# Performance work log

Hardware: AMD Instinct MI355X
Metric: run time of the kernel (lower is better)

Reference implementation:

```python
import jax, jax.numpy as jnp
import numpy as np

T, B, D, H, L = 1024, 64, 512, 512, 2


def setup_inputs() -> dict:
    key = jax.random.key(0)
    ks = jax.random.split(key, 10)
    s = 1.0 / np.sqrt(D)
    return {
        "x": jax.random.normal(ks[0], (T, B, D), jnp.float32),
        "hidden": jax.random.normal(ks[1], (L, B, H), jnp.float32),
        "fc_w": jax.random.normal(ks[2], (D, D), jnp.float32) * s,
        "fc_b": jax.random.normal(ks[3], (D,), jnp.float32) * s,
        "w0": jax.random.normal(ks[4], (H, D), jnp.float32) * s,
        "b0": jax.random.normal(ks[5], (H,), jnp.float32) * s,
        "u0": jax.random.uniform(ks[6], (H,), jnp.float32, -1.0, 1.0),
        "w1": jax.random.normal(ks[7], (H, H), jnp.float32) * s,
        "b1": jax.random.normal(ks[8], (H,), jnp.float32) * s,
        "u1": jax.random.uniform(ks[9], (H,), jnp.float32, -1.0, 1.0),
    }


def _indrnn_layer(inp, h0, w, b, u):
    # Precompute input projection for all timesteps: [T, B, H]
    pre = jnp.einsum("tbd,hd->tbh", inp, w) + b

    def step(h, p):
        h_new = jax.nn.relu(p + u * h)  # elementwise recurrent weight
        return h_new, h_new

    h_last, outs = jax.lax.scan(step, h0, pre)
    return outs, h_last


def reference(x, hidden, fc_w, fc_b, w0, b0, u0, w1, b1, u1):
    # fc layer before the IndRNN stack
    x = jnp.einsum("tbd,ed->tbe", x, fc_w) + fc_b
    out0, h0 = _indrnn_layer(x, hidden[0], w0, b0, u0)
    out1, h1 = _indrnn_layer(out0, hidden[1], w1, b1, u1)
    hn = jnp.stack([h0, h1], axis=0)  # [L, B, H]
    return out1, hn
```

## Files before the change

### kernel.cpp

```cpp
#include <hip/hip_runtime.h>
#include <hip/hip_bf16.h>
#include <cstdint>
#include <cstddef>

#define T_DIM 1024
#define B_DIM 64
#define D_DIM 512
#define H_DIM 512
#define TBROWS (T_DIM * B_DIM)
#define BH (B_DIM * H_DIM)
#define TBH ((size_t)T_DIM * (size_t)BH)

typedef __bf16 bf16x8 __attribute__((ext_vector_type(8)));
typedef float floatx4 __attribute__((ext_vector_type(4)));

__device__ __forceinline__ void async_load16(const void* g, void* l) {
  __builtin_amdgcn_global_load_lds(
      (const __attribute__((address_space(1))) unsigned int*)g,
      (__attribute__((address_space(3))) unsigned int*)l,
      16, 0, 0);
}

__device__ __forceinline__ void wait_vm(int n) {
  switch (n) {
    case 16: asm volatile("s_waitcnt vmcnt(16)" ::: "memory"); break;
    case 24: asm volatile("s_waitcnt vmcnt(24)" ::: "memory"); break;
    case 32: asm volatile("s_waitcnt vmcnt(32)" ::: "memory"); break;
    case 40: asm volatile("s_waitcnt vmcnt(40)" ::: "memory"); break;
    case 48: asm volatile("s_waitcnt vmcnt(48)" ::: "memory"); break;
    default: asm volatile("s_waitcnt vmcnt(0)" ::: "memory"); break;
  }
}

__global__ __launch_bounds__(256) void prep_kernel(
    const float* __restrict__ w0, const float* __restrict__ fc_w,
    const float* __restrict__ fc_b, const float* __restrict__ b0,
    const float* __restrict__ w1, __bf16* __restrict__ Wc,
    __bf16* __restrict__ w1bf, float* __restrict__ bcomb) {
  const int blk = blockIdx.x;
  const int tid = threadIdx.x;
  if (blk < 128) {
    const int h0 = (blk >> 1) * 8;
    const int d = ((blk & 1) << 8) + tid;
    float a[8];
#pragma unroll
    for (int j = 0; j < 8; j++) a[j] = 0.f;
#pragma unroll 4
    for (int e = 0; e < D_DIM; ++e) {
      const float fv = fc_w[(size_t)e * D_DIM + d];
#pragma unroll
      for (int j = 0; j < 8; j++)
        a[j] = fmaf(w0[(size_t)(h0 + j) * D_DIM + e], fv, a[j]);
    }
#pragma unroll
    for (int j = 0; j < 8; j++)
      Wc[(size_t)(h0 + j) * D_DIM + d] = (__bf16)a[j];
  } else if (blk < 256) {
    const long i = ((long)(blk - 128) * 256 + tid) * 8;
    const float4 a = *(const float4*)(w1 + i);
    const float4 b = *(const float4*)(w1 + i + 4);
    bf16x8 v;
    v[0] = (__bf16)a.x; v[1] = (__bf16)a.y; v[2] = (__bf16)a.z; v[3] = (__bf16)a.w;
    v[4] = (__bf16)b.x; v[5] = (__bf16)b.y; v[6] = (__bf16)b.z; v[7] = (__bf16)b.w;
    *(bf16x8*)(w1bf + i) = v;
  } else {
    const int h = (blk - 256) * 256 + tid;
    float acc = b0[h];
    const float4* w4 = (const float4*)(w0 + (size_t)h * D_DIM);
#pragma unroll 4
    for (int e = 0; e < D_DIM / 4; ++e) {
      const float4 wv = w4[e];
      acc = fmaf(wv.x, fc_b[e * 4 + 0], acc);
      acc = fmaf(wv.y, fc_b[e * 4 + 1], acc);
      acc = fmaf(wv.z, fc_b[e * 4 + 2], acc);
      acc = fmaf(wv.w, fc_b[e * 4 + 3], acc);
    }
    bcomb[h] = acc;
  }
}

#define BM 128
#define BN 128
#define BK 32

__device__ __forceinline__ int xcd_swizzle(int bid, int nwg) {
  return (bid & 7) * (nwg >> 3) + (bid >> 3);
}

__global__ __launch_bounds__(256) void gemm_a32_bt_bias(
    const float* __restrict__ A,
    const __bf16* __restrict__ Bm,
    const float* __restrict__ bias,
    __bf16* __restrict__ C,
    int M, int N, int K) {
  __shared__ float Asf[2][BM * BK];
  __shared__ __bf16 Bs[2][BN * BK];

  const int tid = threadIdx.x;
  const int lane = tid & 63;
  const int wave = tid >> 6;
  const int wg = xcd_swizzle((int)blockIdx.x, (int)gridDim.x);
  const int nb = N / BN;
  const int bm = wg / nb;
  const int bn = wg % nb;
  const int m0 = bm * BM, n0 = bn * BN;

  floatx4 zero = {0.f, 0.f, 0.f, 0.f};
  floatx4 acc[4][4];
#pragma unroll
  for (int i = 0; i < 4; i++)
#pragma unroll
    for (int j = 0; j < 4; j++) acc[i][j] = zero;

  const int e0 = (wave * 2 + 0) * 64 + lane;
  const int e1 = (wave * 2 + 1) * 64 + lane;
  const int r0 = e0 >> 2, g0 = (e0 & 3) ^ ((r0 >> 1) & 3);
  const int r1 = e1 >> 2, g1 = (e1 & 3) ^ ((r1 >> 1) & 3);

  const int tm = (wave >> 1) * 64;
  const int tn = (wave & 1) * 64;
  const int lrow = lane & 15;
  const int lk = (lane >> 4) * 8;
  const int sB = lk >> 3;
  const int s0 = lk >> 2;

  const int ea = wave * 4;

  const int KT = K / BK;

  auto stage = [&](int b, int k0) {
#pragma unroll
    for (int i = 0; i < 4; i++) {
      const int e = (ea + i) * 64 + lane;
      const int r = e >> 3;
      const int g = (e & 7) ^ (r & 7);
      async_load16(&A[(size_t)(m0 + r) * K + k0 + g * 4],
                   &Asf[b][(ea + i) * 256]);
    }
    async_load16(&Bm[(size_t)(n0 + r0) * K + k0 + g0 * 8],
                 &Bs[b][(wave * 2 + 0) * 512]);
    async_load16(&Bm[(size_t)(n0 + r1) * K + k0 + g1 * 8],
                 &Bs[b][(wave * 2 + 1) * 512]);
  };

  stage(0, 0);
  __syncthreads();

  int cur = 0;
  for (int kt = 0; kt < KT; ++kt) {
    if (kt + 1 < KT) stage(cur ^ 1, (kt + 1) * BK);

    bf16x8 af[4], bfr[4];
#pragma unroll
    for (int i = 0; i < 4; i++) {
      const int ra = tm + i * 16 + lrow;
      const int k7 = ra & 7;
      const float4 fa = *(const float4*)&Asf[cur][ra * 32 + ((s0 ^ k7) << 2)];
      const float4 fb = *(const float4*)&Asf[cur][ra * 32 + (((s0 + 1) ^ k7) << 2)];
      bf16x8 v;
      v[0] = (__bf16)fa.x; v[1] = (__bf16)fa.y; v[2] = (__bf16)fa.z; v[3] = (__bf16)fa.w;
      v[4] = (__bf16)fb.x; v[5] = (__bf16)fb.y; v[6] = (__bf16)fb.z; v[7] = (__bf16)fb.w;
      af[i] = v;
      const int rb = tn + i * 16 + lrow;
      bfr[i] = *(const bf16x8*)&Bs[cur][rb * 32 + ((sB ^ ((rb >> 1) & 3)) << 3)];
    }
#pragma unroll
    for (int i = 0; i < 4; i++)
#pragma unroll
      for (int j = 0; j < 4; j++)
        acc[i][j] = __builtin_amdgcn_mfma_f32_16x16x32_bf16(af[i], bfr[j],
                                                            acc[i][j], 0, 0, 0);
    __syncthreads();
    cur ^= 1;
  }

  const int ccol = lane & 15;
  const int crow = (lane >> 4) * 4;
  float bv[4];
#pragma unroll
  for (int j = 0; j < 4; j++) bv[j] = bias[n0 + tn + j * 16 + ccol];
#pragma unroll
  for (int i = 0; i < 4; i++) {
#pragma unroll
    for (int j = 0; j < 4; j++) {
      const size_t base =
          (size_t)(m0 + tm + i * 16 + crow) * N + (n0 + tn + j * 16 + ccol);
#pragma unroll
      for (int r = 0; r < 4; r++)
        C[base + (size_t)r * N] = (__bf16)(acc[i][j][r] + bv[j]);
    }
  }
}

__global__ __launch_bounds__(256) void gemm_bt_bias(
    const __bf16* __restrict__ A,
    const __bf16* __restrict__ Bm,
    const float* __restrict__ bias,
    __bf16* __restrict__ C,
    int M, int N, int K) {
  __shared__ __bf16 As[2][BM * BK];
  __shared__ __bf16 Bs[2][BN * BK];

  const int tid = threadIdx.x;
  const int lane = tid & 63;
  const int wave = tid >> 6;
  const int wg = xcd_swizzle((int)blockIdx.x, (int)gridDim.x);
  const int nb = N / BN;
  const int bm = wg / nb;
  const int bn = wg % nb;
  const int m0 = bm * BM, n0 = bn * BN;

  floatx4 zero = {0.f, 0.f, 0.f, 0.f};
  floatx4 acc[4][4];
#pragma unroll
  for (int i = 0; i < 4; i++)
#pragma unroll
    for (int j = 0; j < 4; j++) acc[i][j] = zero;

  const int e0 = (wave * 2 + 0) * 64 + lane;
  const int e1 = (wave * 2 + 1) * 64 + lane;
  const int r0 = e0 >> 2, g0 = (e0 & 3) ^ ((r0 >> 1) & 3);
  const int r1 = e1 >> 2, g1 = (e1 & 3) ^ ((r1 >> 1) & 3);

  const int tm = (wave >> 1) * 64;
  const int tn = (wave & 1) * 64;
  const int lrow = lane & 15;
  const int lk = (lane >> 4) * 8;
  const int sB = lk >> 3;

  const int KT = K / BK;

  auto stage = [&](int b, int k0) {
    async_load16(&A[(size_t)(m0 + r0) * K + k0 + g0 * 8],
                 &As[b][(wave * 2 + 0) * 512]);
    async_load16(&A[(size_t)(m0 + r1) * K + k0 + g1 * 8],
                 &As[b][(wave * 2 + 1) * 512]);
    async_load16(&Bm[(size_t)(n0 + r0) * K + k0 + g0 * 8],
                 &Bs[b][(wave * 2 + 0) * 512]);
    async_load16(&Bm[(size_t)(n0 + r1) * K + k0 + g1 * 8],
                 &Bs[b][(wave * 2 + 1) * 512]);
  };

  stage(0, 0);
  __syncthreads();

  int cur = 0;
  for (int kt = 0; kt < KT; ++kt) {
    if (kt + 1 < KT) stage(cur ^ 1, (kt + 1) * BK);

    bf16x8 af[4], bfr[4];
#pragma unroll
    for (int i = 0; i < 4; i++) {
      const int ra = tm + i * 16 + lrow;
      const int rb = tn + i * 16 + lrow;
      af[i]  = *(const bf16x8*)&As[cur][ra * 32 + ((sB ^ ((ra >> 1) & 3)) << 3)];
      bfr[i] = *(const bf16x8*)&Bs[cur][rb * 32 + ((sB ^ ((rb >> 1) & 3)) << 3)];
    }
#pragma unroll
    for (int i = 0; i < 4; i++)
#pragma unroll
      for (int j = 0; j < 4; j++)
        acc[i][j] = __builtin_amdgcn_mfma_f32_16x16x32_bf16(af[i], bfr[j],
                                                            acc[i][j], 0, 0, 0);
    __syncthreads();
    cur ^= 1;
  }

  const int ccol = lane & 15;
  const int crow = (lane >> 4) * 4;
  float bv[4];
#pragma unroll
  for (int j = 0; j < 4; j++) bv[j] = bias[n0 + tn + j * 16 + ccol];
#pragma unroll
  for (int i = 0; i < 4; i++) {
#pragma unroll
    for (int j = 0; j < 4; j++) {
      const size_t base =
          (size_t)(m0 + tm + i * 16 + crow) * N + (n0 + tn + j * 16 + ccol);
#pragma unroll
      for (int r = 0; r < 4; r++)
        C[base + (size_t)r * N] = (__bf16)(acc[i][j][r] + bv[j]);
    }
  }
}

#define TS 64
#define NTILE (T_DIM / TS)

template <bool BF16OUT>
__global__ __launch_bounds__(64, 1) void scan_kernel(
    const __bf16* __restrict__ pre,
    const float* __restrict__ h0,
    const float* __restrict__ u,
    void* __restrict__ outp,
    float* __restrict__ hn) {
  constexpr int OBYTES = BF16OUT ? 2 : 4;
  __shared__ __bf16 tin[3][TS * 64];
  __shared__ char oraw[2][TS * 64 * OBYTES];

  const int lane = threadIdx.x;
  const int c0 = blockIdx.x * 64;
  const int idx = c0 + lane;
  const float uu = u[idx & (H_DIM - 1)];
  float h = h0[idx];

  const int lrow = lane >> 3;
  const int lcg = (lane & 7) * 8;

#pragma unroll
  for (int i = 0; i < 8; i++)
    async_load16(&pre[(size_t)(i * 8 + lrow) * BH + c0 + lcg], &tin[0][i * 512]);
#pragma unroll
  for (int i = 0; i < 8; i++)
    async_load16(&pre[(size_t)(TS + i * 8 + lrow) * BH + c0 + lcg],
                 &tin[1][i * 512]);

  for (int tile = 0; tile < NTILE; ++tile) {
    __builtin_amdgcn_sched_barrier(0);
    if (tile + 2 < NTILE) {
      const int nb = (tile + 2) % 3;
      const size_t nt0 = (size_t)(tile + 2) * TS;
#pragma unroll
      for (int i = 0; i < 8; i++)
        async_load16(&pre[(nt0 + i * 8 + lrow) * BH + c0 + lcg],
                     &tin[nb][i * 512]);
    }
    int wv;
    if (BF16OUT)
      wv = (tile == 0 || tile == NTILE - 1) ? 16
         : (tile == 1 || tile == NTILE - 2) ? 24 : 32;
    else
      wv = (tile == 0) ? 16
         : (tile == 1 || tile == NTILE - 1) ? 32
         : (tile == NTILE - 2) ? 40 : 48;
    wait_vm(wv);
    __builtin_amdgcn_sched_barrier(0);

    const int buf = tile % 3;
    const int t0 = tile * TS;
    char* ob = oraw[tile & 1];
#pragma unroll
    for (int s = 0; s < TS; s++) {
      const float p = (float)tin[buf][s * 64 + lane];
      h = fmaxf(fmaf(uu, h, p), 0.0f);
      if (BF16OUT) ((__bf16*)ob)[s * 64 + lane] = (__bf16)h;
      else         ((float*)ob)[s * 64 + lane] = h;
    }
    if (BF16OUT) {
#pragma unroll
      for (int i = 0; i < 8; i++) {
        const int row = i * 8 + (lane >> 3);
        const bf16x8 v =
            *(const bf16x8*)&((const __bf16*)ob)[row * 64 + (lane & 7) * 8];
        *(bf16x8*)&((__bf16*)outp)[(size_t)(t0 + row) * BH + c0 + (lane & 7) * 8] = v;
      }
    } else {
#pragma unroll
      for (int i = 0; i < 16; i++) {
        const int row = i * 4 + (lane >> 4);
        const float4 v =
            *(const float4*)&((const float*)ob)[row * 64 + (lane & 15) * 4];
        *(float4*)&((float*)outp)[(size_t)(t0 + row) * BH + c0 + (lane & 15) * 4] = v;
      }
    }
  }
  hn[idx] = h;
}

extern "C" void kernel_launch(void* const* d_in, const int* in_sizes, int n_in,
                              void* d_out, int out_size, void* d_ws,
                              size_t ws_size, hipStream_t stream) {
  (void)in_sizes; (void)n_in; (void)out_size; (void)ws_size;
  const float* x      = (const float*)d_in[0];
  const float* hidden = (const float*)d_in[1];
  const float* fc_w   = (const float*)d_in[2];
  const float* fc_b   = (const float*)d_in[3];
  const float* w0     = (const float*)d_in[4];
  const float* b0     = (const float*)d_in[5];
  const float* u0     = (const float*)d_in[6];
  const float* w1     = (const float*)d_in[7];
  const float* b1     = (const float*)d_in[8];
  const float* u1     = (const float*)d_in[9];
  float* out = (float*)d_out;

  char* ws = (char*)d_ws;
  __bf16* pre  = (__bf16*)ws;
  __bf16* out0 = (__bf16*)(ws + TBH * 2);
  char*   tail = ws + 2 * TBH * 2;
  __bf16* Wc    = (__bf16*)tail;
  __bf16* w1bf  = (__bf16*)(tail + 512 * 1024);
  float*  bcomb = (float*)(tail + 1024 * 1024);

  float* hn = out + TBH;

  prep_kernel<<<258, 256, 0, stream>>>(w0, fc_w, fc_b, b0, w1, Wc, w1bf, bcomb);
  gemm_a32_bt_bias<<<(TBROWS / BM) * (H_DIM / BN), 256, 0, stream>>>(
      x, Wc, bcomb, pre, TBROWS, H_DIM, D_DIM);
  scan_kernel<true><<<BH / 64, 64, 0, stream>>>(pre, hidden, u0, (void*)out0, hn);
  gemm_bt_bias<<<(TBROWS / BM) * (H_DIM / BN), 256, 0, stream>>>(
      out0, w1bf, b1, pre, TBROWS, H_DIM, H_DIM);
  scan_kernel<false><<<BH / 64, 64, 0, stream>>>(pre, hidden + BH, u1,
                                                 (void*)out, hn + BH);
}
```

Measured before the change: 450.7 us.

## Triple-buffer GEMM K-loop with async prefetch depth of two

Both projection GEMMs move from double to triple buffering in LDS. Tiles are prefetched two iterations ahead, and partial s_waitcnt vmcnt counts let the newest loads stay in flight while the current tile is consumed. Raw s_barrier plus sched_barrier replace __syncthreads so the compiler cannot reorder around the waits. This adds LDS use, which can lower occupancy (fp32 A tiles now need 48KB+24KB), and it relies on hand-set vmcnt values being correct.

```diff
diff --git a/kernel.cpp b/kernel.cpp
--- a/kernel.cpp
+++ b/kernel.cpp
@@ -23,12 +23,16 @@
 
 __device__ __forceinline__ void wait_vm(int n) {
   switch (n) {
+    case 4:  asm volatile("s_waitcnt vmcnt(4)"  ::: "memory"); break;
+    case 6:  asm volatile("s_waitcnt vmcnt(6)"  ::: "memory"); break;
+    case 8:  asm volatile("s_waitcnt vmcnt(8)"  ::: "memory"); break;
+    case 12: asm volatile("s_waitcnt vmcnt(12)" ::: "memory"); break;
     case 16: asm volatile("s_waitcnt vmcnt(16)" ::: "memory"); break;
     case 24: asm volatile("s_waitcnt vmcnt(24)" ::: "memory"); break;
     case 32: asm volatile("s_waitcnt vmcnt(32)" ::: "memory"); break;
     case 40: asm volatile("s_waitcnt vmcnt(40)" ::: "memory"); break;
     case 48: asm volatile("s_waitcnt vmcnt(48)" ::: "memory"); break;
-    default: asm volatile("s_waitcnt vmcnt(0)" ::: "memory"); break;
+    default: asm volatile("s_waitcnt vmcnt(0)"  ::: "memory"); break;
   }
 }
 
@@ -93,8 +97,8 @@
     const float* __restrict__ bias,
     __bf16* __restrict__ C,
     int M, int N, int K) {
-  __shared__ float Asf[2][BM * BK];
-  __shared__ __bf16 Bs[2][BN * BK];
+  __shared__ float Asf[3][BM * BK];
+  __shared__ __bf16 Bs[3][BN * BK];
 
   const int tid = threadIdx.x;
   const int lane = tid & 63;
@@ -128,7 +132,8 @@
 
   const int KT = K / BK;
 
-  auto stage = [&](int b, int k0) {
+  auto stage = [&](int b, int kt) {
+    const int k0 = kt * BK;
 #pragma unroll
     for (int i = 0; i < 4; i++) {
       const int e = (ea + i) * 64 + lane;
@@ -144,25 +149,29 @@
   };
 
   stage(0, 0);
-  __syncthreads();
-
-  int cur = 0;
-  for (int kt = 0; kt < KT; ++kt) {
-    if (kt + 1 < KT) stage(cur ^ 1, (kt + 1) * BK);
-
+  stage(1, 1);
+  stage(2, 2);
+
+  for (int t = 0; t < KT; ++t) {
+    const int rem = KT - 1 - t;
+    wait_vm(rem >= 2 ? 12 : (rem == 1 ? 6 : 0));
+    __builtin_amdgcn_s_barrier();
+    __builtin_amdgcn_sched_barrier(0);
+
+    const int buf = t % 3;
     bf16x8 af[4], bfr[4];
 #pragma unroll
     for (int i = 0; i < 4; i++) {
       const int ra = tm + i * 16 + lrow;
       const int k7 = ra & 7;
-      const float4 fa = *(const float4*)&Asf[cur][ra * 32 + ((s0 ^ k7) << 2)];
-      const float4 fb = *(const float4*)&Asf[cur][ra * 32 + (((s0 + 1) ^ k7) << 2)];
+      const float4 fa = *(const float4*)&Asf[buf][ra * 32 + ((s0 ^ k7) << 2)];
+      const float4 fb = *(const float4*)&Asf[buf][ra * 32 + (((s0 + 1) ^ k7) << 2)];
       bf16x8 v;
       v[0] = (__bf16)fa.x; v[1] = (__bf16)fa.y; v[2] = (__bf16)fa.z; v[3] = (__bf16)fa.w;
       v[4] = (__bf16)fb.x; v[5] = (__bf16)fb.y; v[6] = (__bf16)fb.z; v[7] = (__bf16)fb.w;
       af[i] = v;
       const int rb = tn + i * 16 + lrow;
-      bfr[i] = *(const bf16x8*)&Bs[cur][rb * 32 + ((sB ^ ((rb >> 1) & 3)) << 3)];
+      bfr[i] = *(const bf16x8*)&Bs[buf][rb * 32 + ((sB ^ ((rb >> 1) & 3)) << 3)];
     }
 #pragma unroll
     for (int i = 0; i < 4; i++)
@@ -170,8 +179,10 @@
       for (int j = 0; j < 4; j++)
         acc[i][j] = __builtin_amdgcn_mfma_f32_16x16x32_bf16(af[i], bfr[j],
                                                             acc[i][j], 0, 0, 0);
-    __syncthreads();
-    cur ^= 1;
+    __builtin_amdgcn_sched_barrier(0);
+    __builtin_amdgcn_s_barrier();
+    __builtin_amdgcn_sched_barrier(0);
+    if (t + 3 < KT) stage(buf, t + 3);
   }
 
   const int ccol = lane & 15;
@@ -198,8 +209,8 @@
     const float* __restrict__ bias,
     __bf16* __restrict__ C,
     int M, int N, int K) {
-  __shared__ __bf16 As[2][BM * BK];
-  __shared__ __bf16 Bs[2][BN * BK];
+  __shared__ __bf16 As[3][BM * BK];
+  __shared__ __bf16 Bs[3][BN * BK];
 
   const int tid = threadIdx.x;
   const int lane = tid & 63;
@@ -230,7 +241,8 @@
 
   const int KT = K / BK;
 
-  auto stage = [&](int b, int k0) {
+  auto stage = [&](int b, int kt) {
+    const int k0 = kt * BK;
     async_load16(&A[(size_t)(m0 + r0) * K + k0 + g0 * 8],
                  &As[b][(wave * 2 + 0) * 512]);
     async_load16(&A[(size_t)(m0 + r1) * K + k0 + g1 * 8],
@@ -242,19 +254,23 @@
   };
 
   stage(0, 0);
-  __syncthreads();
-
-  int cur = 0;
-  for (int kt = 0; kt < KT; ++kt) {
-    if (kt + 1 < KT) stage(cur ^ 1, (kt + 1) * BK);
-
+  stage(1, 1);
+  stage(2, 2);
+
+  for (int t = 0; t < KT; ++t) {
+    const int rem = KT - 1 - t;
+    wait_vm(rem >= 2 ? 8 : (rem == 1 ? 4 : 0));
+    __builtin_amdgcn_s_barrier();
+    __builtin_amdgcn_sched_barrier(0);
+
+    const int buf = t % 3;
     bf16x8 af[4], bfr[4];
 #pragma unroll
     for (int i = 0; i < 4; i++) {
       const int ra = tm + i * 16 + lrow;
       const int rb = tn + i * 16 + lrow;
-      af[i]  = *(const bf16x8*)&As[cur][ra * 32 + ((sB ^ ((ra >> 1) & 3)) << 3)];
-      bfr[i] = *(const bf16x8*)&Bs[cur][rb * 32 + ((sB ^ ((rb >> 1) & 3)) << 3)];
+      af[i]  = *(const bf16x8*)&As[buf][ra * 32 + ((sB ^ ((ra >> 1) & 3)) << 3)];
+      bfr[i] = *(const bf16x8*)&Bs[buf][rb * 32 + ((sB ^ ((rb >> 1) & 3)) << 3)];
     }
 #pragma unroll
     for (int i = 0; i < 4; i++)
@@ -262,8 +278,10 @@
       for (int j = 0; j < 4; j++)
         acc[i][j] = __builtin_amdgcn_mfma_f32_16x16x32_bf16(af[i], bfr[j],
                                                             acc[i][j], 0, 0, 0);
-    __syncthreads();
-    cur ^= 1;
+    __builtin_amdgcn_sched_barrier(0);
+    __builtin_amdgcn_s_barrier();
+    __builtin_amdgcn_sched_barrier(0);
+    if (t + 3 < KT) stage(buf, t + 3);
   }
 
   const int ccol = lane & 15;
```

Result: slower. 468.9 us (+4.0%).
